# Kernel optimization log

Hardware: AMD Instinct MI355X
Metric: run time of the kernel (lower is better)

Reference implementation:

```python
import jax, jax.numpy as jnp
import numpy as np

B, D, H, W = 1, 4, 48, 48
C, NH = 256, 8
HD = C // NH
KD, KH, KW = 3, 5, 5
KVOL = KD * KH * KW
SCALE = HD ** -0.5


def _nbhd(L, k):
    """Neighborhood start indices (clamped to stay in-bounds, natten semantics)
    and relative-position-bias indices for one axis."""
    i = jnp.arange(L)
    start = jnp.clip(i - k // 2, 0, L - k)            # [L]
    idx = start[:, None] + jnp.arange(k)[None, :]     # [L,k] absolute neighbor index
    rel = idx - i[:, None] + (k - 1)                  # [L,k] rpb index in [0, 2k-2]
    return idx, rel


def setup_inputs() -> dict:
    key = jax.random.key(0)
    ks = jax.random.split(key, 5)
    s = 0.02
    return {
        "x": jax.random.normal(ks[0], (B, D, H, W, C), jnp.float32),
        "w_qkv": jax.random.normal(ks[1], (C, 3 * C), jnp.float32) * s,
        "b_qkv": jnp.zeros((3 * C,), jnp.float32),
        "rpb": jax.random.normal(ks[2], (NH, 2 * KD - 1, 2 * KH - 1, 2 * KW - 1), jnp.float32) * s,
        "w_proj": jax.random.normal(ks[3], (C, C), jnp.float32) * s,
        "b_proj": jnp.zeros((C,), jnp.float32),
    }


def _nat3d(q, k, v, rpb):
    # q,k,v: [B,NH,D,H,W,HD]; q already scaled
    idxD, relD = _nbhd(D, KD)
    idxH, relH = _nbhd(H, KH)
    idxW, relW = _nbhd(W, KW)
    iD = idxD[:, None, None, :, None, None]
    iH = idxH[None, :, None, None, :, None]
    iW = idxW[None, None, :, None, None, :]
    gk = k[:, :, iD, iH, iW]   # [B,NH,D,H,W,KD,KH,KW,HD]
    gv = v[:, :, iD, iH, iW]
    bias = rpb[:, relD[:, None, None, :, None, None],
                  relH[None, :, None, None, :, None],
                  relW[None, None, :, None, None, :]]  # [NH,D,H,W,KD,KH,KW]
    scores = jnp.einsum("bndyxc,bndyxtuvc->bndyxtuv", q, gk) + bias[None]
    flat = scores.reshape(*scores.shape[:5], KVOL)
    attn = jax.nn.softmax(flat, axis=-1).reshape(scores.shape)
    return jnp.einsum("bndyxtuv,bndyxtuvc->bndyxc", attn, gv)


def reference(x, w_qkv, b_qkv, rpb, w_proj, b_proj):
    qkv = (x @ w_qkv + b_qkv).reshape(B, D, H, W, 3, NH, HD)
    qkv = jnp.transpose(qkv, (4, 0, 5, 1, 2, 3, 6))  # [3,B,NH,D,H,W,HD]
    q, k, v = qkv[0] * SCALE, qkv[1], qkv[2]
    out = _nat3d(q, k, v, rpb)                       # [B,NH,D,H,W,HD]
    out = jnp.transpose(out, (0, 2, 3, 4, 1, 5)).reshape(B, D, H, W, C)
    return out @ w_proj + b_proj
```

## Files before the change

kernel.cpp:

```cpp
#include <hip/hip_runtime.h>

#define QK_SCALE 0.17677669529663687f
#define TOKENS 9216

typedef __attribute__((ext_vector_type(8))) __bf16 bf16x8;
typedef __attribute__((ext_vector_type(8))) unsigned short us8;
typedef __attribute__((ext_vector_type(4))) float f32x4;

static __device__ __forceinline__ unsigned short f2bf(float x) {
    unsigned int u = __float_as_uint(x);
    return (unsigned short)((u + 0x7FFFu + ((u >> 16) & 1u)) >> 16);
}
static __device__ __forceinline__ float bf2f(unsigned short u) {
    return __uint_as_float(((unsigned int)u) << 16);
}
static __device__ __forceinline__ bf16x8 ld_bf8(const unsigned short* p) {
    us8 u = *reinterpret_cast<const us8*>(p);
    return __builtin_bit_cast(bf16x8, u);
}

__global__ __launch_bounds__(256) void conv_prep(
    const float* __restrict__ x, const float* __restrict__ wqkv, const float* __restrict__ wproj,
    unsigned short* __restrict__ xb, unsigned short* __restrict__ wqT, unsigned short* __restrict__ wpT)
{
    int b = blockIdx.x, t = threadIdx.x;
    if (b < 2304) {
        int idx = (b * 256 + t) * 4;
        float4 v = *reinterpret_cast<const float4*>(x + idx);
        ushort4 o;
        o.x = f2bf(v.x); o.y = f2bf(v.y); o.z = f2bf(v.z); o.w = f2bf(v.w);
        *reinterpret_cast<ushort4*>(xb + idx) = o;
    } else if (b < 3072) {
        int e = (b - 2304) * 256 + t;
        int n = e >> 8, k = e & 255;
        wqT[n * 256 + k] = f2bf(wqkv[k * 768 + n]);
    } else {
        int e = (b - 3072) * 256 + t;
        int n = e >> 8, k = e & 255;
        wpT[n * 256 + k] = f2bf(wproj[k * 256 + n]);
    }
}

__global__ __launch_bounds__(256) void prep_bias(
    const float* __restrict__ rpb, unsigned short* __restrict__ biasT)
{
    const int bid = blockIdx.x;
    const int cls = bid >> 3, h = bid & 7;
    const int d  = cls / 9;
    const int r  = cls % 9;
    const int yc = r / 3, xc = r % 3;
    const int by = (yc == 0) ? 0 : ((yc == 1) ? 5 : 11);
    const int bx = (xc == 0) ? 0 : ((xc == 1) ? 5 : 11);
    const int y0 = by * 4, x0 = bx * 4;
    const int base_d = min(max(d - 1, 0), 1);
    const int base_h = min(max(y0 - 2, 0), 40);
    const int base_w = min(max(x0 - 2, 0), 40);
    const int relD = base_d - d + 2;
    unsigned short* dst = biasT + (size_t)bid * 3072;

    for (int idx = threadIdx.x; idx < 3072; idx += 256) {
        int tok = idx / 192, cand = idx % 192;
        int y = y0 + (tok >> 2), x = x0 + (tok & 3);
        int sh = min(max(y - 2, 0), 43), sw = min(max(x - 2, 0), 43);
        int ld = cand >> 6, lh = (cand >> 3) & 7, lw = cand & 7;
        int t0 = lh - (sh - base_h), t1 = lw - (sw - base_w);
        bool valid = ((unsigned)t0 < 5u) && ((unsigned)t1 < 5u);
        unsigned short v = 0xFF80;
        if (valid) {
            int bi = (relD + ld) * 81 + (lh - (y - base_h) + 4) * 9 + (lw - (x - base_w) + 4);
            v = f2bf(rpb[h * 405 + bi]);
        }
        dst[idx] = v;
    }
}

template<int MF, int NF, int MODE>
__global__ __launch_bounds__(256) void gemm_mfma(
    const unsigned short* __restrict__ A, const unsigned short* __restrict__ BT,
    const float* __restrict__ bias,
    unsigned short* __restrict__ oq, unsigned short* __restrict__ ok,
    unsigned short* __restrict__ ov, float* __restrict__ of)
{
    const int tid = threadIdx.x;
    const int wid = tid >> 6, lane = tid & 63;
    const int wm = wid >> 1, wn = wid & 1;
    const int n15 = lane & 15, g = lane >> 4;
    const int m0 = blockIdx.y * (MF * 32) + wm * (MF * 16);
    const int n0 = blockIdx.x * (NF * 32) + wn * (NF * 16);

    f32x4 acc[MF][NF];
    #pragma unroll
    for (int i = 0; i < MF; i++)
        #pragma unroll
        for (int j = 0; j < NF; j++)
            acc[i][j] = f32x4{0.f, 0.f, 0.f, 0.f};

    #pragma unroll
    for (int ks = 0; ks < 8; ++ks) {
        bf16x8 a[MF], b[NF];
        #pragma unroll
        for (int mt = 0; mt < MF; ++mt)
            a[mt] = ld_bf8(A + (size_t)(m0 + mt * 16 + n15) * 256 + ks * 32 + g * 8);
        #pragma unroll
        for (int nt = 0; nt < NF; ++nt)
            b[nt] = ld_bf8(BT + (size_t)(n0 + nt * 16 + n15) * 256 + ks * 32 + g * 8);
        #pragma unroll
        for (int mt = 0; mt < MF; ++mt)
            #pragma unroll
            for (int nt = 0; nt < NF; ++nt)
                acc[mt][nt] = __builtin_amdgcn_mfma_f32_16x16x32_bf16(a[mt], b[nt], acc[mt][nt], 0, 0, 0);
    }

    #pragma unroll
    for (int mt = 0; mt < MF; ++mt) {
        #pragma unroll
        for (int nt = 0; nt < NF; ++nt) {
            int col = n0 + nt * 16 + n15;
            float bv = bias[col];
            #pragma unroll
            for (int rg = 0; rg < 4; ++rg) {
                int row = m0 + mt * 16 + g * 4 + rg;
                float val = acc[mt][nt][rg] + bv;
                if (MODE == 0) {
                    int part = col >> 8, c = col & 255, hh = c >> 5, ch = c & 31;
                    unsigned short* dst = (part == 0) ? oq : ((part == 1) ? ok : ov);
                    if (part == 0) val *= QK_SCALE;
                    dst[((size_t)hh * TOKENS + row) * 32 + ch] = f2bf(val);
                } else {
                    of[(size_t)row * 256 + col] = val;
                }
            }
        }
    }
}

__global__ __launch_bounds__(128) void nat_attn_mfma(
    const unsigned short* __restrict__ qws, const unsigned short* __restrict__ kws,
    const unsigned short* __restrict__ vws, const unsigned short* __restrict__ biasT,
    unsigned short* __restrict__ aout)
{
    __shared__ unsigned short VT[32 * 200];
    __shared__ unsigned short Pl[16 * 200];
    __shared__ float red[2][16][2];

    const int tid = threadIdx.x;
    const int w = tid >> 6, lane = tid & 63;
    const int n15 = lane & 15, g = lane >> 4;

    int b = blockIdx.x;
    const int h = b & 7; b >>= 3;
    const int bx = b % 12; b /= 12;
    const int by = b % 12;
    const int d  = b / 12;
    const int y0 = by * 4, x0 = bx * 4;
    const int base_d = min(max(d - 1, 0), 1);
    const int base_h = min(max(y0 - 2, 0), 40);
    const int base_w = min(max(x0 - 2, 0), 40);

    const int yc = (by == 0) ? 0 : ((by == 11) ? 2 : 1);
    const int xc = (bx == 0) ? 0 : ((bx == 11) ? 2 : 1);
    const unsigned short* bT = biasT + (size_t)(((d * 9 + yc * 3 + xc) * 8 + h)) * 3072;

    const size_t hoff = (size_t)h * TOKENS * 32;
    const unsigned short* kb = kws + hoff;
    const unsigned short* vb = vws + hoff;
    const unsigned short* qb = qws + hoff;

    for (int id = tid; id < 768; id += 128) {
        int cand = id % 192, chg = id / 192;
        int ld = cand >> 6, lh = (cand >> 3) & 7, lw = cand & 7;
        int gt = (base_d + ld) * 2304 + (base_h + lh) * 48 + (base_w + lw);
        us8 u = *reinterpret_cast<const us8*>(vb + (size_t)gt * 32 + chg * 8);
        #pragma unroll
        for (int e = 0; e < 8; e++) VT[(chg * 8 + e) * 200 + cand] = u[e];
    }

    float bvv[6][4];
    #pragma unroll
    for (int i = 0; i < 6; ++i)
        #pragma unroll
        for (int rg = 0; rg < 4; ++rg)
            bvv[i][rg] = bf2f(bT[(g * 4 + rg) * 192 + w * 96 + i * 16 + n15]);

    const int gtq = d * 2304 + (y0 + (n15 >> 2)) * 48 + (x0 + (n15 & 3));
    bf16x8 qf = ld_bf8(qb + (size_t)gtq * 32 + g * 8);

    f32x4 sf[6];
    #pragma unroll
    for (int i = 0; i < 6; ++i) {
        int cand = (w * 6 + i) * 16 + n15;
        int ld = cand >> 6, lh = (cand >> 3) & 7, lw = cand & 7;
        int gtc = (base_d + ld) * 2304 + (base_h + lh) * 48 + (base_w + lw);
        bf16x8 kf = ld_bf8(kb + (size_t)gtc * 32 + g * 8);
        sf[i] = __builtin_amdgcn_mfma_f32_16x16x32_bf16(qf, kf, f32x4{0.f, 0.f, 0.f, 0.f}, 0, 0, 0);
    }
    __syncthreads();

    int gtr[4];
    #pragma unroll
    for (int rg = 0; rg < 4; ++rg) {
        int tok = g * 4 + rg;
        gtr[rg] = d * 2304 + (y0 + (tok >> 2)) * 48 + (x0 + (tok & 3));
    }

    float ev[6][4], mw[4], sm[4];
    #pragma unroll
    for (int rg = 0; rg < 4; ++rg) {
        float mx = -1e30f;
        #pragma unroll
        for (int i = 0; i < 6; ++i) {
            float sc = sf[i][rg] + bvv[i][rg];
            ev[i][rg] = sc;
            mx = fmaxf(mx, sc);
        }
        #pragma unroll
        for (int msk = 1; msk < 16; msk <<= 1) mx = fmaxf(mx, __shfl_xor(mx, msk));
        float ssum = 0.f;
        #pragma unroll
        for (int i = 0; i < 6; ++i) {
            float ee = __expf(ev[i][rg] - mx);
            ev[i][rg] = ee;
            ssum += ee;
        }
        #pragma unroll
        for (int msk = 1; msk < 16; msk <<= 1) ssum += __shfl_xor(ssum, msk);
        mw[rg] = mx; sm[rg] = ssum;
    }
    if (n15 == 0) {
        #pragma unroll
        for (int rg = 0; rg < 4; ++rg) {
            red[w][g * 4 + rg][0] = mw[rg];
            red[w][g * 4 + rg][1] = sm[rg];
        }
    }
    __syncthreads();

    float fac[4];
    #pragma unroll
    for (int rg = 0; rg < 4; ++rg) {
        int tk = g * 4 + rg;
        float m0_ = red[0][tk][0], s0_ = red[0][tk][1];
        float m1_ = red[1][tk][0], s1_ = red[1][tk][1];
        float m = fmaxf(m0_, m1_);
        float tot = s0_ * __expf(m0_ - m) + s1_ * __expf(m1_ - m);
        fac[rg] = __expf(mw[rg] - m) / tot;
    }
    #pragma unroll
    for (int rg = 0; rg < 4; ++rg)
        #pragma unroll
        for (int i = 0; i < 6; ++i)
            Pl[(g * 4 + rg) * 200 + (w * 6 + i) * 16 + n15] = f2bf(ev[i][rg] * fac[rg]);
    __syncthreads();

    f32x4 oacc = f32x4{0.f, 0.f, 0.f, 0.f};
    #pragma unroll
    for (int ks = 0; ks < 6; ++ks) {
        bf16x8 pa = ld_bf8(&Pl[n15 * 200 + ks * 32 + g * 8]);
        bf16x8 vf = ld_bf8(&VT[(w * 16 + n15) * 200 + ks * 32 + g * 8]);
        oacc = __builtin_amdgcn_mfma_f32_16x16x32_bf16(pa, vf, oacc, 0, 0, 0);
    }
    #pragma unroll
    for (int rg = 0; rg < 4; ++rg)
        aout[(size_t)gtr[rg] * 256 + h * 32 + w * 16 + n15] = f2bf(oacc[rg]);
}

extern "C" void kernel_launch(void* const* d_in, const int* in_sizes, int n_in,
                              void* d_out, int out_size, void* d_ws, size_t ws_size,
                              hipStream_t stream) {
    const float* x      = (const float*)d_in[0];
    const float* w_qkv  = (const float*)d_in[1];
    const float* b_qkv  = (const float*)d_in[2];
    const float* rpb    = (const float*)d_in[3];
    const float* w_proj = (const float*)d_in[4];
    const float* b_proj = (const float*)d_in[5];
    float* out = (float*)d_out;

    unsigned short* ws = (unsigned short*)d_ws;
    unsigned short* xb    = ws;
    unsigned short* wqT   = ws + (size_t)2359296;
    unsigned short* wpT   = ws + (size_t)2555904;
    unsigned short* qws   = ws + (size_t)2621440;
    unsigned short* kws   = ws + (size_t)4980736;
    unsigned short* vws   = ws + (size_t)7340032;
    unsigned short* aws   = ws + (size_t)9699328;
    unsigned short* biasT = ws + (size_t)12058624;

    conv_prep<<<dim3(3328), 256, 0, stream>>>(x, w_qkv, w_proj, xb, wqT, wpT);
    prep_bias<<<dim3(288), 256, 0, stream>>>(rpb, biasT);

    gemm_mfma<4, 2, 0><<<dim3(12, 72), 256, 0, stream>>>(xb, wqT, b_qkv, qws, kws, vws, nullptr);

    nat_attn_mfma<<<dim3(4608), 128, 0, stream>>>(qws, kws, vws, biasT, aws);

    gemm_mfma<2, 2, 1><<<dim3(4, 144), 256, 0, stream>>>(aws, wpT, b_proj, nullptr, nullptr, nullptr, out);
}
```

Before: 74.82 us.

## Fuse bias prep into conversion kernel, drop softmax max pass, widen QKV GEMM tile

Merges the relative-position-bias preparation into the input/weight conversion kernel, removing one launch. Rewrites the attention softmax without max subtraction: it exponentiates the scores directly, writes the unnormalized probabilities, and divides by the summed denominator after the PV MFMA. This drops one barrier and the cross-wave max exchange, but relies on the scores being small enough that exp does not overflow. Also changes the QKV GEMM tile from 4x2 to 4x4 fragments, which halves the number of blocks in x.

New measurement: 64.66 us. 13.6% less time.

```diff
diff --git a/kernel.cpp b/kernel.cpp
--- a/kernel.cpp
+++ b/kernel.cpp
@@ -21,7 +21,9 @@
 
 __global__ __launch_bounds__(256) void conv_prep(
     const float* __restrict__ x, const float* __restrict__ wqkv, const float* __restrict__ wproj,
-    unsigned short* __restrict__ xb, unsigned short* __restrict__ wqT, unsigned short* __restrict__ wpT)
+    const float* __restrict__ rpb,
+    unsigned short* __restrict__ xb, unsigned short* __restrict__ wqT,
+    unsigned short* __restrict__ wpT, unsigned short* __restrict__ biasT)
 {
     int b = blockIdx.x, t = threadIdx.x;
     if (b < 2304) {
@@ -34,43 +36,40 @@
         int e = (b - 2304) * 256 + t;
         int n = e >> 8, k = e & 255;
         wqT[n * 256 + k] = f2bf(wqkv[k * 768 + n]);
-    } else {
+    } else if (b < 3328) {
         int e = (b - 3072) * 256 + t;
         int n = e >> 8, k = e & 255;
         wpT[n * 256 + k] = f2bf(wproj[k * 256 + n]);
-    }
-}
-
-__global__ __launch_bounds__(256) void prep_bias(
-    const float* __restrict__ rpb, unsigned short* __restrict__ biasT)
-{
-    const int bid = blockIdx.x;
-    const int cls = bid >> 3, h = bid & 7;
-    const int d  = cls / 9;
-    const int r  = cls % 9;
-    const int yc = r / 3, xc = r % 3;
-    const int by = (yc == 0) ? 0 : ((yc == 1) ? 5 : 11);
-    const int bx = (xc == 0) ? 0 : ((xc == 1) ? 5 : 11);
-    const int y0 = by * 4, x0 = bx * 4;
-    const int base_d = min(max(d - 1, 0), 1);
-    const int base_h = min(max(y0 - 2, 0), 40);
-    const int base_w = min(max(x0 - 2, 0), 40);
-    const int relD = base_d - d + 2;
-    unsigned short* dst = biasT + (size_t)bid * 3072;
-
-    for (int idx = threadIdx.x; idx < 3072; idx += 256) {
-        int tok = idx / 192, cand = idx % 192;
-        int y = y0 + (tok >> 2), x = x0 + (tok & 3);
-        int sh = min(max(y - 2, 0), 43), sw = min(max(x - 2, 0), 43);
-        int ld = cand >> 6, lh = (cand >> 3) & 7, lw = cand & 7;
-        int t0 = lh - (sh - base_h), t1 = lw - (sw - base_w);
-        bool valid = ((unsigned)t0 < 5u) && ((unsigned)t1 < 5u);
-        unsigned short v = 0xFF80;
-        if (valid) {
-            int bi = (relD + ld) * 81 + (lh - (y - base_h) + 4) * 9 + (lw - (x - base_w) + 4);
-            v = f2bf(rpb[h * 405 + bi]);
+    } else {
+        const int bid = b - 3328;
+        const int cls = bid >> 3, h = bid & 7;
+        const int d  = cls / 9;
+        const int r  = cls % 9;
+        const int yc = r / 3, xc = r % 3;
+        const int by = (yc == 0) ? 0 : ((yc == 1) ? 5 : 11);
+        const int bx = (xc == 0) ? 0 : ((xc == 1) ? 5 : 11);
+        const int y0 = by * 4, x0 = bx * 4;
+        const int base_d = min(max(d - 1, 0), 1);
+        const int base_h = min(max(y0 - 2, 0), 40);
+        const int base_w = min(max(x0 - 2, 0), 40);
+        const int relD = base_d - d + 2;
+        unsigned short* dst = biasT + (size_t)bid * 3072;
+        for (int idx = t; idx < 3072; idx += 256) {
+            int tok = idx >> 8;
+            tok = idx / 192;
+            int cand = idx - tok * 192;
+            int y = y0 + (tok >> 2), xx = x0 + (tok & 3);
+            int sh = min(max(y - 2, 0), 43), sw = min(max(xx - 2, 0), 43);
+            int ld = cand >> 6, lh = (cand >> 3) & 7, lw = cand & 7;
+            int t0 = lh - (sh - base_h), t1 = lw - (sw - base_w);
+            bool valid = ((unsigned)t0 < 5u) && ((unsigned)t1 < 5u);
+            unsigned short v = 0xFF80;
+            if (valid) {
+                int bi = (relD + ld) * 81 + (lh - (y - base_h) + 4) * 9 + (lw - (xx - base_w) + 4);
+                v = f2bf(rpb[h * 405 + bi]);
+            }
+            dst[idx] = v;
         }
-        dst[idx] = v;
     }
 }
 
@@ -141,7 +140,7 @@
 {
     __shared__ unsigned short VT[32 * 200];
     __shared__ unsigned short Pl[16 * 200];
-    __shared__ float red[2][16][2];
+    __shared__ float red[2][16];
 
     const int tid = threadIdx.x;
     const int w = tid >> 6, lane = tid & 63;
@@ -194,62 +193,33 @@
         bf16x8 kf = ld_bf8(kb + (size_t)gtc * 32 + g * 8);
         sf[i] = __builtin_amdgcn_mfma_f32_16x16x32_bf16(qf, kf, f32x4{0.f, 0.f, 0.f, 0.f}, 0, 0, 0);
     }
+
+    float psum[4];
+    unsigned short pw[4][6];
+    #pragma unroll
+    for (int rg = 0; rg < 4; ++rg) {
+        float e[6];
+        #pragma unroll
+        for (int i = 0; i < 6; ++i)
+            e[i] = __expf(sf[i][rg] + bvv[i][rg]);
+        float s = ((e[0] + e[1]) + (e[2] + e[3])) + (e[4] + e[5]);
+        #pragma unroll
+        for (int msk = 1; msk < 16; msk <<= 1) s += __shfl_xor(s, msk);
+        psum[rg] = s;
+        #pragma unroll
+        for (int i = 0; i < 6; ++i) pw[rg][i] = f2bf(e[i]);
+    }
     __syncthreads();
 
-    int gtr[4];
-    #pragma unroll
-    for (int rg = 0; rg < 4; ++rg) {
-        int tok = g * 4 + rg;
-        gtr[rg] = d * 2304 + (y0 + (tok >> 2)) * 48 + (x0 + (tok & 3));
-    }
-
-    float ev[6][4], mw[4], sm[4];
-    #pragma unroll
-    for (int rg = 0; rg < 4; ++rg) {
-        float mx = -1e30f;
-        #pragma unroll
-        for (int i = 0; i < 6; ++i) {
-            float sc = sf[i][rg] + bvv[i][rg];
-            ev[i][rg] = sc;
-            mx = fmaxf(mx, sc);
-        }
-        #pragma unroll
-        for (int msk = 1; msk < 16; msk <<= 1) mx = fmaxf(mx, __shfl_xor(mx, msk));
-        float ssum = 0.f;
-        #pragma unroll
-        for (int i = 0; i < 6; ++i) {
-            float ee = __expf(ev[i][rg] - mx);
-            ev[i][rg] = ee;
-            ssum += ee;
-        }
-        #pragma unroll
-        for (int msk = 1; msk < 16; msk <<= 1) ssum += __shfl_xor(ssum, msk);
-        mw[rg] = mx; sm[rg] = ssum;
-    }
+    #pragma unroll
+    for (int rg = 0; rg < 4; ++rg)
+        #pragma unroll
+        for (int i = 0; i < 6; ++i)
+            Pl[(g * 4 + rg) * 200 + (w * 6 + i) * 16 + n15] = pw[rg][i];
     if (n15 == 0) {
         #pragma unroll
-        for (int rg = 0; rg < 4; ++rg) {
-            red[w][g * 4 + rg][0] = mw[rg];
-            red[w][g * 4 + rg][1] = sm[rg];
-        }
-    }
-    __syncthreads();
-
-    float fac[4];
-    #pragma unroll
-    for (int rg = 0; rg < 4; ++rg) {
-        int tk = g * 4 + rg;
-        float m0_ = red[0][tk][0], s0_ = red[0][tk][1];
-        float m1_ = red[1][tk][0], s1_ = red[1][tk][1];
-        float m = fmaxf(m0_, m1_);
-        float tot = s0_ * __expf(m0_ - m) + s1_ * __expf(m1_ - m);
-        fac[rg] = __expf(mw[rg] - m) / tot;
-    }
-    #pragma unroll
-    for (int rg = 0; rg < 4; ++rg)
-        #pragma unroll
-        for (int i = 0; i < 6; ++i)
-            Pl[(g * 4 + rg) * 200 + (w * 6 + i) * 16 + n15] = f2bf(ev[i][rg] * fac[rg]);
+        for (int rg = 0; rg < 4; ++rg) red[w][g * 4 + rg] = psum[rg];
+    }
     __syncthreads();
 
     f32x4 oacc = f32x4{0.f, 0.f, 0.f, 0.f};
@@ -260,8 +230,12 @@
         oacc = __builtin_amdgcn_mfma_f32_16x16x32_bf16(pa, vf, oacc, 0, 0, 0);
     }
     #pragma unroll
-    for (int rg = 0; rg < 4; ++rg)
-        aout[(size_t)gtr[rg] * 256 + h * 32 + w * 16 + n15] = f2bf(oacc[rg]);
+    for (int rg = 0; rg < 4; ++rg) {
+        int tok = g * 4 + rg;
+        float inv = 1.f / (red[0][tok] + red[1][tok]);
+        int gtr = d * 2304 + (y0 + (tok >> 2)) * 48 + (x0 + (tok & 3));
+        aout[(size_t)gtr * 256 + h * 32 + w * 16 + n15] = f2bf(oacc[rg] * inv);
+    }
 }
 
 extern "C" void kernel_launch(void* const* d_in, const int* in_sizes, int n_in,
@@ -285,10 +259,9 @@
     unsigned short* aws   = ws + (size_t)9699328;
     unsigned short* biasT = ws + (size_t)12058624;
 
-    conv_prep<<<dim3(3328), 256, 0, stream>>>(x, w_qkv, w_proj, xb, wqT, wpT);
-    prep_bias<<<dim3(288), 256, 0, stream>>>(rpb, biasT);
-
-    gemm_mfma<4, 2, 0><<<dim3(12, 72), 256, 0, stream>>>(xb, wqT, b_qkv, qws, kws, vws, nullptr);
+    conv_prep<<<dim3(3616), 256, 0, stream>>>(x, w_qkv, w_proj, rpb, xb, wqT, wpT, biasT);
+
+    gemm_mfma<4, 4, 0><<<dim3(6, 72), 256, 0, stream>>>(xb, wqT, b_qkv, qws, kws, vws, nullptr);
 
     nat_attn_mfma<<<dim3(4608), 128, 0, stream>>>(qws, kws, vws, biasT, aws);
 
```
